# Optimization experiments

Hardware: AMD Instinct MI355X
Metric: run time of the kernel (lower is better)

The kernel has to match this reference:

```python
import jax, jax.numpy as jnp
import numpy as np

H = 1024      # hidden_size
V = 50257     # output_size (vocab)
L = 40        # max_length (attention span)
NL = 2        # num_layers


def setup_inputs() -> dict:
    key = jax.random.key(0)
    ks = jax.random.split(key, 20)
    s = 0.02
    f32 = jnp.float32
    d = {
        "input_token": jax.random.randint(ks[0], (1,), 0, V),
        "h0": jax.random.normal(ks[1], (NL, 1, H), f32),
        "c0": jax.random.normal(ks[2], (NL, 1, H), f32),
        "encoder_outputs": jax.random.normal(ks[3], (L, 2 * H), f32),
        # parameters (PyTorch Linear convention: y = x @ W.T + b)
        "emb": jax.random.normal(ks[4], (V, H), f32) * s,
        "attn_w": jax.random.normal(ks[5], (L, (NL + 1) * H), f32) * s,
        "attn_b": jnp.zeros((L,), f32),
        "comb_w": jax.random.normal(ks[6], (H, 3 * H), f32) * s,
        "comb_b": jnp.zeros((H,), f32),
        "w_ih0": jax.random.normal(ks[7], (4 * H, H), f32) * s,
        "w_hh0": jax.random.normal(ks[8], (4 * H, H), f32) * s,
        "b_ih0": jnp.zeros((4 * H,), f32),
        "b_hh0": jnp.zeros((4 * H,), f32),
        "w_ih1": jax.random.normal(ks[9], (4 * H, H), f32) * s,
        "w_hh1": jax.random.normal(ks[10], (4 * H, H), f32) * s,
        "b_ih1": jnp.zeros((4 * H,), f32),
        "b_hh1": jnp.zeros((4 * H,), f32),
        "out_w": jax.random.normal(ks[11], (V, H), f32) * s,
        "out_b": jnp.zeros((V,), f32),
    }
    return d


def _lstm_cell(x, h, c, w_ih, w_hh, b_ih, b_hh):
    # PyTorch gate order: i, f, g, o
    g = x @ w_ih.T + b_ih + h @ w_hh.T + b_hh  # [1, 4H]
    i, f, gg, o = jnp.split(g, 4, axis=-1)
    c2 = jax.nn.sigmoid(f) * c + jax.nn.sigmoid(i) * jnp.tanh(gg)
    h2 = jax.nn.sigmoid(o) * jnp.tanh(c2)
    return h2, c2


def reference(input_token, h0, c0, encoder_outputs, emb, attn_w, attn_b,
              comb_w, comb_b, w_ih0, w_hh0, b_ih0, b_hh0, w_ih1, w_hh1,
              b_ih1, b_hh1, out_w, out_b):
    embedded = emb[input_token]  # [1, H] (dropout is identity in eval)
    # attention over encoder positions: input = [embedded ; flattened h]
    attn_in = jnp.concatenate([embedded, h0.reshape(1, -1)], axis=1)  # [1, 3H]
    attn_weights = jax.nn.softmax(attn_in @ attn_w.T + attn_b, axis=1)  # [1, L]
    attn_applied = attn_weights @ encoder_outputs  # [1, 2H]
    x = jnp.concatenate([embedded, attn_applied], axis=1) @ comb_w.T + comb_b
    x = jax.nn.relu(x)  # [1, H]
    # 2-layer LSTM, single time step
    h_l0, c_l0 = _lstm_cell(x, h0[0], c0[0], w_ih0, w_hh0, b_ih0, b_hh0)
    h_l1, c_l1 = _lstm_cell(h_l0, h0[1], c0[1], w_ih1, w_hh1, b_ih1, b_hh1)
    h_new = jnp.stack([h_l0, h_l1])  # [NL, 1, H]
    c_new = jnp.stack([c_l0, c_l1])
    log_probs = jax.nn.log_softmax(h_l1 @ out_w.T + out_b, axis=1)  # [1, V]
    return (log_probs, h_new, c_new, attn_weights)
```

## Files before the change

### kernel.cpp

```cpp
#include <hip/hip_runtime.h>
#include <cmath>

#define H 1024
#define VOCAB 50257
#define LSPAN 40

__device__ inline float wave_reduce(float v) {
    for (int o = 32; o > 0; o >>= 1) v += __shfl_down(v, o, 64);
    return v;
}

__global__ void attn_logits_k(const int* __restrict__ tok,
                              const float* __restrict__ h0,
                              const float* __restrict__ emb,
                              const float* __restrict__ attn_w,
                              const float* __restrict__ attn_b,
                              float* __restrict__ ws_logits,
                              float* __restrict__ ws_xin) {
    const int l = blockIdx.x;
    const int t = threadIdx.x;
    const float* __restrict__ er = emb + (size_t)tok[0] * H;
    const float4* __restrict__ w4 = (const float4*)(attn_w + (size_t)l * 3 * H);
    const float4* __restrict__ e4 = (const float4*)er;
    const float4* __restrict__ h4 = (const float4*)h0;
    float acc = 0.f;
    for (int k = t; k < 768; k += 256) {
        float4 w = w4[k];
        float4 x = (k < 256) ? e4[k] : h4[k - 256];
        acc += w.x * x.x + w.y * x.y + w.z * x.z + w.w * x.w;
    }
    if (l == 0 && t < 256) {
        ((float4*)ws_xin)[t] = e4[t];
    }
    __shared__ float lds[4];
    float s = wave_reduce(acc);
    const int wave = t >> 6, lane = t & 63;
    if (lane == 0) lds[wave] = s;
    __syncthreads();
    if (t == 0) ws_logits[l] = lds[0] + lds[1] + lds[2] + lds[3] + attn_b[l];
}

__global__ void attn_apply_k(const float* __restrict__ ws_logits,
                             const float* __restrict__ enc,
                             float* __restrict__ ws_xin,
                             float* __restrict__ out_attnw) {
    __shared__ float lg[LSPAN];
    const int t = threadIdx.x;
    if (t < LSPAN) lg[t] = ws_logits[t];
    __syncthreads();
    float m = -1e30f;
    for (int l = 0; l < LSPAN; ++l) m = fmaxf(m, lg[l]);
    float denom = 0.f;
    for (int l = 0; l < LSPAN; ++l) denom += expf(lg[l] - m);
    const int j = blockIdx.x * 256 + t;
    float acc = 0.f;
    for (int l = 0; l < LSPAN; ++l) {
        acc += expf(lg[l] - m) * enc[l * 2 * H + j];
    }
    ws_xin[H + j] = acc / denom;
    if (blockIdx.x == 0 && t < LSPAN) out_attnw[t] = expf(lg[t] - m) / denom;
}

__global__ void comb_k(const float* __restrict__ ws_xin,
                       const float* __restrict__ comb_w,
                       const float* __restrict__ comb_b,
                       float* __restrict__ ws_x) {
    const int wave = threadIdx.x >> 6, lane = threadIdx.x & 63;
    const int r = blockIdx.x * 4 + wave;
    const float4* __restrict__ w4 = (const float4*)(comb_w + (size_t)r * 3 * H);
    const float4* __restrict__ x4 = (const float4*)ws_xin;
    float acc = 0.f;
    for (int k = lane; k < 768; k += 64) {
        float4 a = w4[k], b = x4[k];
        acc += a.x * b.x + a.y * b.y + a.z * b.z + a.w * b.w;
    }
    acc = wave_reduce(acc);
    if (lane == 0) ws_x[r] = fmaxf(acc + comb_b[r], 0.f);
}

__global__ void lstm_k(const float* __restrict__ x,
                       const float* __restrict__ hprev,
                       const float* __restrict__ cprev,
                       const float* __restrict__ w_ih,
                       const float* __restrict__ w_hh,
                       const float* __restrict__ b_ih,
                       const float* __restrict__ b_hh,
                       float* __restrict__ h_out,
                       float* __restrict__ c_out) {
    const int wave = threadIdx.x >> 6, lane = threadIdx.x & 63;
    const int j = blockIdx.x;
    const int row = wave * H + j;
    const float4* __restrict__ wi4 = (const float4*)(w_ih + (size_t)row * H);
    const float4* __restrict__ wh4 = (const float4*)(w_hh + (size_t)row * H);
    const float4* __restrict__ x4 = (const float4*)x;
    const float4* __restrict__ h4 = (const float4*)hprev;
    float acc = 0.f;
    for (int k = lane; k < 256; k += 64) {
        float4 a = wi4[k], b = x4[k];
        acc += a.x * b.x + a.y * b.y + a.z * b.z + a.w * b.w;
        float4 c = wh4[k], d = h4[k];
        acc += c.x * d.x + c.y * d.y + c.z * d.z + c.w * d.w;
    }
    acc = wave_reduce(acc);
    __shared__ float g[4];
    if (lane == 0) g[wave] = acc + b_ih[row] + b_hh[row];
    __syncthreads();
    if (threadIdx.x == 0) {
        const float i = g[0], f = g[1], gg = g[2], o = g[3];
        const float si = 1.f / (1.f + expf(-i));
        const float sf = 1.f / (1.f + expf(-f));
        const float so = 1.f / (1.f + expf(-o));
        const float c2 = sf * cprev[j] + si * tanhf(gg);
        const float h2 = so * tanhf(c2);
        c_out[j] = c2;
        h_out[j] = h2;
    }
}

__global__ void out_gemv_k(const float* __restrict__ hvec,
                           const float* __restrict__ out_w,
                           const float* __restrict__ out_b,
                           float* __restrict__ logits,
                           float* __restrict__ stats) {
    __shared__ float4 h4s[256];
    const int t = threadIdx.x;
    h4s[t] = ((const float4*)hvec)[t];
    __syncthreads();
    const int wave = t >> 6, lane = t & 63;
    const int v = blockIdx.x * 4 + wave;
    float val = -1e30f;
    if (v < VOCAB) {
        const float4* __restrict__ w4 = (const float4*)(out_w + (size_t)v * H);
        float acc = 0.f;
        for (int k = lane; k < 256; k += 64) {
            float4 a = w4[k];
            float4 b = h4s[k];
            acc += a.x * b.x + a.y * b.y + a.z * b.z + a.w * b.w;
        }
        acc = wave_reduce(acc);
        val = acc + out_b[v];
    }
    __shared__ float g[4];
    if (lane == 0) {
        g[wave] = val;
        if (v < VOCAB) logits[v] = val;
    }
    __syncthreads();
    if (t == 0) {
        float m = fmaxf(fmaxf(g[0], g[1]), fmaxf(g[2], g[3]));
        float s = 0.f;
        for (int w = 0; w < 4; ++w)
            if (g[w] > -1e29f) s += expf(g[w] - m);
        stats[2 * blockIdx.x] = m;
        stats[2 * blockIdx.x + 1] = s;
    }
}

__global__ void logz_k(const float* __restrict__ stats, int nblocks,
                       float* __restrict__ logz) {
    const int t = threadIdx.x;
    float M = -1e30f, S = 0.f;
    for (int b = t; b < nblocks; b += 256) {
        const float m = stats[2 * b], s = stats[2 * b + 1];
        if (m > M) { S = S * expf(M - m) + s; M = m; }
        else       { S += s * expf(m - M); }
    }
    __shared__ float Ms[256], Ss[256];
    Ms[t] = M; Ss[t] = S;
    __syncthreads();
    for (int stride = 128; stride > 0; stride >>= 1) {
        if (t < stride) {
            const float m1 = Ms[t], s1 = Ss[t];
            const float m2 = Ms[t + stride], s2 = Ss[t + stride];
            const float mm = fmaxf(m1, m2);
            Ms[t] = mm;
            Ss[t] = s1 * expf(m1 - mm) + s2 * expf(m2 - mm);
        }
        __syncthreads();
    }
    if (t == 0) logz[0] = Ms[0] + logf(Ss[0]);
}

__global__ void finalize_k(float* __restrict__ logits,
                           const float* __restrict__ logz) {
    const int v = blockIdx.x * 256 + threadIdx.x;
    if (v < VOCAB) logits[v] -= logz[0];
}

extern "C" void kernel_launch(void* const* d_in, const int* in_sizes, int n_in,
                              void* d_out, int out_size, void* d_ws, size_t ws_size,
                              hipStream_t stream) {
    const int*   tok    = (const int*)d_in[0];
    const float* h0     = (const float*)d_in[1];
    const float* c0     = (const float*)d_in[2];
    const float* enc    = (const float*)d_in[3];
    const float* emb    = (const float*)d_in[4];
    const float* attn_w = (const float*)d_in[5];
    const float* attn_b = (const float*)d_in[6];
    const float* comb_w = (const float*)d_in[7];
    const float* comb_b = (const float*)d_in[8];
    const float* w_ih0  = (const float*)d_in[9];
    const float* w_hh0  = (const float*)d_in[10];
    const float* b_ih0  = (const float*)d_in[11];
    const float* b_hh0  = (const float*)d_in[12];
    const float* w_ih1  = (const float*)d_in[13];
    const float* w_hh1  = (const float*)d_in[14];
    const float* b_ih1  = (const float*)d_in[15];
    const float* b_hh1  = (const float*)d_in[16];
    const float* out_w  = (const float*)d_in[17];
    const float* out_b  = (const float*)d_in[18];

    float* out = (float*)d_out;
    float* ws  = (float*)d_ws;

    float* ws_xin    = ws;
    float* ws_x      = ws + 3072;
    float* ws_logits = ws + 4096;
    float* ws_logz   = ws + 4160;
    float* ws_stats  = ws + 4224;

    float* out_logp  = out;
    float* out_h     = out + VOCAB;
    float* out_c     = out + VOCAB + 2 * H;
    float* out_attnw = out + VOCAB + 4 * H;

    attn_logits_k<<<LSPAN, 256, 0, stream>>>(tok, h0, emb, attn_w, attn_b,
                                             ws_logits, ws_xin);
    attn_apply_k<<<8, 256, 0, stream>>>(ws_logits, enc, ws_xin, out_attnw);
    comb_k<<<256, 256, 0, stream>>>(ws_xin, comb_w, comb_b, ws_x);
    lstm_k<<<H, 256, 0, stream>>>(ws_x, h0, c0, w_ih0, w_hh0, b_ih0, b_hh0,
                                  out_h, out_c);
    lstm_k<<<H, 256, 0, stream>>>(out_h, h0 + H, c0 + H, w_ih1, w_hh1, b_ih1,
                                  b_hh1, out_h + H, out_c + H);
    const int NB5 = (VOCAB + 3) / 4;
    out_gemv_k<<<NB5, 256, 0, stream>>>(out_h + H, out_w, out_b, out_logp,
                                        ws_stats);
    logz_k<<<1, 256, 0, stream>>>(ws_stats, NB5, ws_logz);
    finalize_k<<<(VOCAB + 255) / 256, 256, 0, stream>>>(out_logp, ws_logz);
}
```

Measured before the change: 481.0 us.

## Fuse all decoder stages into one cooperative persistent kernel with grid syncs

Replaces the sequence of separate kernel launches (attention logits, attention apply, combine, two LSTM layers, output GEMV, log-softmax) with a single cooperative kernel of 1024 blocks that separates the stages with grid.sync(). The output projection also folds an online max/sum-exp merge into the GEMV, so the log-softmax normalization needs only one extra pass over the logits. The aim is to remove per-launch overhead and inter-kernel gaps. The cost is grid-wide barriers and many idle blocks in the small stages. The old multi-kernel path remains as a fallback if the cooperative launch fails.

```diff
diff --git a/kernel.cpp b/kernel.cpp
--- a/kernel.cpp
+++ b/kernel.cpp
@@ -1,14 +1,196 @@
 #include <hip/hip_runtime.h>
+#include <hip/hip_cooperative_groups.h>
 #include <cmath>
+
+namespace cg = cooperative_groups;
 
 #define H 1024
 #define VOCAB 50257
 #define LSPAN 40
-
-__device__ inline float wave_reduce(float v) {
+#define GRID 1024
+#define NTHR 256
+
+__device__ __forceinline__ float wave_reduce(float v) {
     for (int o = 32; o > 0; o >>= 1) v += __shfl_down(v, o, 64);
     return v;
 }
+
+__device__ __forceinline__ void lsm_merge(float& M, float& S, float m, float s) {
+    if (m > M) { S = S * expf(M - m) + s; M = m; }
+    else       { S += s * expf(m - M); }
+}
+
+__device__ __forceinline__ void lstm_cell(
+    const int j, const int wave, const int lane, const int tid,
+    const float* __restrict__ x, const float* __restrict__ hprev,
+    const float* __restrict__ cprev,
+    const float* __restrict__ w_ih, const float* __restrict__ w_hh,
+    const float* __restrict__ b_ih, const float* __restrict__ b_hh,
+    float* __restrict__ h_out, float* __restrict__ c_out,
+    float* sred) {
+    const int row = wave * H + j;
+    const float4* __restrict__ wi4 = (const float4*)(w_ih + (size_t)row * H);
+    const float4* __restrict__ wh4 = (const float4*)(w_hh + (size_t)row * H);
+    const float4* __restrict__ x4 = (const float4*)x;
+    const float4* __restrict__ h4 = (const float4*)hprev;
+    float acc = 0.f;
+    for (int k = lane; k < 256; k += 64) {
+        float4 a = wi4[k], b = x4[k];
+        acc += a.x * b.x + a.y * b.y + a.z * b.z + a.w * b.w;
+        float4 c = wh4[k], d = h4[k];
+        acc += c.x * d.x + c.y * d.y + c.z * d.z + c.w * d.w;
+    }
+    acc = wave_reduce(acc);
+    if (lane == 0) sred[wave] = acc + b_ih[row] + b_hh[row];
+    __syncthreads();
+    if (tid == 0) {
+        const float i = sred[0], f = sred[1], gg = sred[2], o = sred[3];
+        const float si = 1.f / (1.f + expf(-i));
+        const float sf = 1.f / (1.f + expf(-f));
+        const float so = 1.f / (1.f + expf(-o));
+        const float c2 = sf * cprev[j] + si * tanhf(gg);
+        c_out[j] = c2;
+        h_out[j] = so * tanhf(c2);
+    }
+}
+
+__global__ __launch_bounds__(NTHR, 4) void mega_k(
+    const int* __restrict__ tok, const float* __restrict__ h0,
+    const float* __restrict__ c0, const float* __restrict__ enc,
+    const float* __restrict__ emb, const float* __restrict__ attn_w,
+    const float* __restrict__ attn_b, const float* __restrict__ comb_w,
+    const float* __restrict__ comb_b,
+    const float* __restrict__ w_ih0, const float* __restrict__ w_hh0,
+    const float* __restrict__ b_ih0, const float* __restrict__ b_hh0,
+    const float* __restrict__ w_ih1, const float* __restrict__ w_hh1,
+    const float* __restrict__ b_ih1, const float* __restrict__ b_hh1,
+    const float* __restrict__ out_w, const float* __restrict__ out_b,
+    float* __restrict__ out, float* __restrict__ ws) {
+    cg::grid_group grid = cg::this_grid();
+    const int bid = blockIdx.x, tid = threadIdx.x;
+    const int wave = tid >> 6, lane = tid & 63;
+
+    float* ws_xin   = ws;
+    float* ws_x     = ws + 3072;
+    float* ws_lg    = ws + 4096;
+    float* ws_stats = ws + 4224;
+
+    float* out_logp  = out;
+    float* out_h     = out + VOCAB;
+    float* out_c     = out + VOCAB + 2 * H;
+    float* out_attnw = out + VOCAB + 4 * H;
+
+    __shared__ float4 sh4[256];
+    __shared__ float sA[256];
+    __shared__ float sB[256];
+    __shared__ float slg[LSPAN];
+
+    if (bid < LSPAN) {
+        const float* __restrict__ er = emb + (size_t)tok[0] * H;
+        const float4* __restrict__ w4 = (const float4*)(attn_w + (size_t)bid * 3 * H);
+        const float4* __restrict__ e4 = (const float4*)er;
+        const float4* __restrict__ h4 = (const float4*)h0;
+        float acc = 0.f;
+        for (int k = tid; k < 768; k += NTHR) {
+            float4 w = w4[k];
+            float4 x = (k < 256) ? e4[k] : h4[k - 256];
+            acc += w.x * x.x + w.y * x.y + w.z * x.z + w.w * x.w;
+        }
+        if (bid == 0) ((float4*)ws_xin)[tid] = e4[tid];
+        float s = wave_reduce(acc);
+        if (lane == 0) sA[wave] = s;
+        __syncthreads();
+        if (tid == 0) ws_lg[bid] = sA[0] + sA[1] + sA[2] + sA[3] + attn_b[bid];
+    }
+    grid.sync();
+
+    if (bid < 8) {
+        if (tid < LSPAN) slg[tid] = ws_lg[tid];
+        __syncthreads();
+        float m = -1e30f;
+        for (int l = 0; l < LSPAN; ++l) m = fmaxf(m, slg[l]);
+        float denom = 0.f;
+        for (int l = 0; l < LSPAN; ++l) denom += expf(slg[l] - m);
+        const int j = bid * NTHR + tid;
+        float acc = 0.f;
+        for (int l = 0; l < LSPAN; ++l) acc += expf(slg[l] - m) * enc[l * 2 * H + j];
+        ws_xin[H + j] = acc / denom;
+        if (bid == 0 && tid < LSPAN) out_attnw[tid] = expf(slg[tid] - m) / denom;
+    }
+    grid.sync();
+
+    if (bid < 256) {
+        const int r = bid * 4 + wave;
+        const float4* __restrict__ w4 = (const float4*)(comb_w + (size_t)r * 3 * H);
+        const float4* __restrict__ x4 = (const float4*)ws_xin;
+        float acc = 0.f;
+        for (int k = lane; k < 768; k += 64) {
+            float4 a = w4[k], b = x4[k];
+            acc += a.x * b.x + a.y * b.y + a.z * b.z + a.w * b.w;
+        }
+        acc = wave_reduce(acc);
+        if (lane == 0) ws_x[r] = fmaxf(acc + comb_b[r], 0.f);
+    }
+    grid.sync();
+
+    lstm_cell(bid, wave, lane, tid, ws_x, h0, c0, w_ih0, w_hh0, b_ih0, b_hh0,
+              out_h, out_c, sA);
+    grid.sync();
+
+    lstm_cell(bid, wave, lane, tid, out_h, h0 + H, c0 + H, w_ih1, w_hh1, b_ih1,
+              b_hh1, out_h + H, out_c + H, sA);
+    grid.sync();
+
+    sh4[tid] = ((const float4*)(out_h + H))[tid];
+    __syncthreads();
+    float M = -1e30f, S = 0.f;
+    for (int v = bid * 4 + wave; v < VOCAB; v += GRID * 4) {
+        const float4* __restrict__ w4 = (const float4*)(out_w + (size_t)v * H);
+        float acc = 0.f;
+        #pragma unroll
+        for (int k = lane; k < 256; k += 64) {
+            float4 a = w4[k];
+            float4 b = sh4[k];
+            acc += a.x * b.x + a.y * b.y + a.z * b.z + a.w * b.w;
+        }
+        acc = wave_reduce(acc);
+        if (lane == 0) {
+            const float val = acc + out_b[v];
+            out_logp[v] = val;
+            lsm_merge(M, S, val, 1.f);
+        }
+    }
+    if (lane == 0) { sA[wave] = M; sB[wave] = S; }
+    __syncthreads();
+    if (tid == 0) {
+        float Mb = sA[0], Sb = sB[0];
+        for (int w = 1; w < 4; ++w) lsm_merge(Mb, Sb, sA[w], sB[w]);
+        ws_stats[2 * bid] = Mb;
+        ws_stats[2 * bid + 1] = Sb;
+    }
+    grid.sync();
+
+    float M2 = -1e30f, S2 = 0.f;
+    for (int b = tid; b < GRID; b += NTHR)
+        lsm_merge(M2, S2, ws_stats[2 * b], ws_stats[2 * b + 1]);
+    sA[tid] = M2;
+    sB[tid] = S2;
+    __syncthreads();
+    for (int stride = 128; stride > 0; stride >>= 1) {
+        if (tid < stride) {
+            const float m1 = sA[tid], s1 = sB[tid];
+            const float m2 = sA[tid + stride], s2 = sB[tid + stride];
+            const float mm = fmaxf(m1, m2);
+            sA[tid] = mm;
+            sB[tid] = s1 * expf(m1 - mm) + s2 * expf(m2 - mm);
+        }
+        __syncthreads();
+    }
+    const float logZ = sA[0] + logf(sB[0]);
+    for (int v = bid * NTHR + tid; v < VOCAB; v += GRID * NTHR)
+        out_logp[v] -= logZ;
+}
+
 
 __global__ void attn_logits_k(const int* __restrict__ tok,
                               const float* __restrict__ h0,
@@ -29,9 +211,7 @@
         float4 x = (k < 256) ? e4[k] : h4[k - 256];
         acc += w.x * x.x + w.y * x.y + w.z * x.z + w.w * x.w;
     }
-    if (l == 0 && t < 256) {
-        ((float4*)ws_xin)[t] = e4[t];
-    }
+    if (l == 0 && t < 256) ((float4*)ws_xin)[t] = e4[t];
     __shared__ float lds[4];
     float s = wave_reduce(acc);
     const int wave = t >> 6, lane = t & 63;
@@ -54,9 +234,7 @@
     for (int l = 0; l < LSPAN; ++l) denom += expf(lg[l] - m);
     const int j = blockIdx.x * 256 + t;
     float acc = 0.f;
-    for (int l = 0; l < LSPAN; ++l) {
-        acc += expf(lg[l] - m) * enc[l * 2 * H + j];
-    }
+    for (int l = 0; l < LSPAN; ++l) acc += expf(lg[l] - m) * enc[l * 2 * H + j];
     ws_xin[H + j] = acc / denom;
     if (blockIdx.x == 0 && t < LSPAN) out_attnw[t] = expf(lg[t] - m) / denom;
 }
@@ -88,33 +266,9 @@
                        float* __restrict__ h_out,
                        float* __restrict__ c_out) {
     const int wave = threadIdx.x >> 6, lane = threadIdx.x & 63;
-    const int j = blockIdx.x;
-    const int row = wave * H + j;
-    const float4* __restrict__ wi4 = (const float4*)(w_ih + (size_t)row * H);
-    const float4* __restrict__ wh4 = (const float4*)(w_hh + (size_t)row * H);
-    const float4* __restrict__ x4 = (const float4*)x;
-    const float4* __restrict__ h4 = (const float4*)hprev;
-    float acc = 0.f;
-    for (int k = lane; k < 256; k += 64) {
-        float4 a = wi4[k], b = x4[k];
-        acc += a.x * b.x + a.y * b.y + a.z * b.z + a.w * b.w;
-        float4 c = wh4[k], d = h4[k];
-        acc += c.x * d.x + c.y * d.y + c.z * d.z + c.w * d.w;
-    }
-    acc = wave_reduce(acc);
     __shared__ float g[4];
-    if (lane == 0) g[wave] = acc + b_ih[row] + b_hh[row];
-    __syncthreads();
-    if (threadIdx.x == 0) {
-        const float i = g[0], f = g[1], gg = g[2], o = g[3];
-        const float si = 1.f / (1.f + expf(-i));
-        const float sf = 1.f / (1.f + expf(-f));
-        const float so = 1.f / (1.f + expf(-o));
-        const float c2 = sf * cprev[j] + si * tanhf(gg);
-        const float h2 = so * tanhf(c2);
-        c_out[j] = c2;
-        h_out[j] = h2;
-    }
+    lstm_cell(blockIdx.x, wave, lane, threadIdx.x, x, hprev, cprev, w_ih, w_hh,
+              b_ih, b_hh, h_out, c_out, g);
 }
 
 __global__ void out_gemv_k(const float* __restrict__ hvec,
@@ -213,6 +367,16 @@
     float* out = (float*)d_out;
     float* ws  = (float*)d_ws;
 
+    void* params[] = {
+        (void*)&tok, (void*)&h0, (void*)&c0, (void*)&enc, (void*)&emb,
+        (void*)&attn_w, (void*)&attn_b, (void*)&comb_w, (void*)&comb_b,
+        (void*)&w_ih0, (void*)&w_hh0, (void*)&b_ih0, (void*)&b_hh0,
+        (void*)&w_ih1, (void*)&w_hh1, (void*)&b_ih1, (void*)&b_hh1,
+        (void*)&out_w, (void*)&out_b, (void*)&out, (void*)&ws};
+    hipError_t err = hipLaunchCooperativeKernel((const void*)mega_k, dim3(GRID),
+                                                dim3(NTHR), params, 0, stream);
+    if (err == hipSuccess) return;
+
     float* ws_xin    = ws;
     float* ws_x      = ws + 3072;
     float* ws_logits = ws + 4096;
```

Measured after the change: 1.135 ms. 2.36x slower.

## Fuse attention kernels and merge logsumexp reduction into finalize kernel

Applied to the files above, without the earlier changes.

Merges the attention-logit and attention-apply kernels into one kernel, where each of the 8 blocks recomputes all 40 logits redundantly with one wave per row. The vocab GEMV now uses 1024-thread blocks covering 16 rows, with an online max/sum merge per block. The separate logz kernel is folded into finalize: every one of 50 blocks re-reduces all per-block stats before subtracting. This cuts the launch count from 8 to 6 in exchange for redundant recomputation inside blocks.

```diff
diff --git a/kernel.cpp b/kernel.cpp
--- a/kernel.cpp
+++ b/kernel.cpp
@@ -4,61 +4,55 @@
 #define H 1024
 #define VOCAB 50257
 #define LSPAN 40
-
-__device__ inline float wave_reduce(float v) {
+#define NB5 3142
+#define NBF 50
+
+__device__ __forceinline__ float wave_reduce(float v) {
     for (int o = 32; o > 0; o >>= 1) v += __shfl_down(v, o, 64);
     return v;
 }
 
-__global__ void attn_logits_k(const int* __restrict__ tok,
-                              const float* __restrict__ h0,
-                              const float* __restrict__ emb,
-                              const float* __restrict__ attn_w,
-                              const float* __restrict__ attn_b,
-                              float* __restrict__ ws_logits,
-                              float* __restrict__ ws_xin) {
-    const int l = blockIdx.x;
-    const int t = threadIdx.x;
+__device__ __forceinline__ void lsm_merge(float& M, float& S, float m, float s) {
+    if (m > M) { S = S * expf(M - m) + s; M = m; }
+    else       { S += s * expf(m - M); }
+}
+
+__global__ void attn_k(const int* __restrict__ tok,
+                       const float* __restrict__ h0,
+                       const float* __restrict__ emb,
+                       const float* __restrict__ attn_w,
+                       const float* __restrict__ attn_b,
+                       const float* __restrict__ enc,
+                       float* __restrict__ ws_xin,
+                       float* __restrict__ out_attnw) {
+    const int t = threadIdx.x, bid = blockIdx.x;
+    const int wave = t >> 6, lane = t & 63;
+    __shared__ float slg[LSPAN];
     const float* __restrict__ er = emb + (size_t)tok[0] * H;
-    const float4* __restrict__ w4 = (const float4*)(attn_w + (size_t)l * 3 * H);
     const float4* __restrict__ e4 = (const float4*)er;
     const float4* __restrict__ h4 = (const float4*)h0;
+    for (int l = wave; l < LSPAN; l += 4) {
+        const float4* __restrict__ w4 = (const float4*)(attn_w + (size_t)l * 3 * H);
+        float acc = 0.f;
+        for (int k = lane; k < 768; k += 64) {
+            float4 w = w4[k];
+            float4 x = (k < 256) ? e4[k] : h4[k - 256];
+            acc += w.x * x.x + w.y * x.y + w.z * x.z + w.w * x.w;
+        }
+        acc = wave_reduce(acc);
+        if (lane == 0) slg[l] = acc + attn_b[l];
+    }
+    if (bid == 0) ((float4*)ws_xin)[t] = e4[t];
+    __syncthreads();
+    float m = -1e30f;
+    for (int l = 0; l < LSPAN; ++l) m = fmaxf(m, slg[l]);
+    float denom = 0.f;
+    for (int l = 0; l < LSPAN; ++l) denom += expf(slg[l] - m);
+    const int j = bid * 256 + t;
     float acc = 0.f;
-    for (int k = t; k < 768; k += 256) {
-        float4 w = w4[k];
-        float4 x = (k < 256) ? e4[k] : h4[k - 256];
-        acc += w.x * x.x + w.y * x.y + w.z * x.z + w.w * x.w;
-    }
-    if (l == 0 && t < 256) {
-        ((float4*)ws_xin)[t] = e4[t];
-    }
-    __shared__ float lds[4];
-    float s = wave_reduce(acc);
-    const int wave = t >> 6, lane = t & 63;
-    if (lane == 0) lds[wave] = s;
-    __syncthreads();
-    if (t == 0) ws_logits[l] = lds[0] + lds[1] + lds[2] + lds[3] + attn_b[l];
-}
-
-__global__ void attn_apply_k(const float* __restrict__ ws_logits,
-                             const float* __restrict__ enc,
-                             float* __restrict__ ws_xin,
-                             float* __restrict__ out_attnw) {
-    __shared__ float lg[LSPAN];
-    const int t = threadIdx.x;
-    if (t < LSPAN) lg[t] = ws_logits[t];
-    __syncthreads();
-    float m = -1e30f;
-    for (int l = 0; l < LSPAN; ++l) m = fmaxf(m, lg[l]);
-    float denom = 0.f;
-    for (int l = 0; l < LSPAN; ++l) denom += expf(lg[l] - m);
-    const int j = blockIdx.x * 256 + t;
-    float acc = 0.f;
-    for (int l = 0; l < LSPAN; ++l) {
-        acc += expf(lg[l] - m) * enc[l * 2 * H + j];
-    }
+    for (int l = 0; l < LSPAN; ++l) acc += expf(slg[l] - m) * enc[l * 2 * H + j];
     ws_xin[H + j] = acc / denom;
-    if (blockIdx.x == 0 && t < LSPAN) out_attnw[t] = expf(lg[t] - m) / denom;
+    if (bid == 0 && t < LSPAN) out_attnw[t] = expf(slg[t] - m) / denom;
 }
 
 __global__ void comb_k(const float* __restrict__ ws_xin,
@@ -117,74 +111,74 @@
     }
 }
 
-__global__ void out_gemv_k(const float* __restrict__ hvec,
-                           const float* __restrict__ out_w,
-                           const float* __restrict__ out_b,
-                           float* __restrict__ logits,
-                           float* __restrict__ stats) {
-    __shared__ float4 h4s[256];
+__global__ __launch_bounds__(1024, 2) void out_gemv_k(
+    const float* __restrict__ hvec,
+    const float* __restrict__ out_w,
+    const float* __restrict__ out_b,
+    float* __restrict__ logits,
+    float* __restrict__ stats) {
+    __shared__ float4 sh4[256];
+    __shared__ float sM[16], sS[16];
     const int t = threadIdx.x;
-    h4s[t] = ((const float4*)hvec)[t];
+    if (t < 256) sh4[t] = ((const float4*)hvec)[t];
     __syncthreads();
     const int wave = t >> 6, lane = t & 63;
-    const int v = blockIdx.x * 4 + wave;
-    float val = -1e30f;
+    const int v = blockIdx.x * 16 + wave;
+    float M = -1e30f, S = 0.f;
     if (v < VOCAB) {
         const float4* __restrict__ w4 = (const float4*)(out_w + (size_t)v * H);
         float acc = 0.f;
-        for (int k = lane; k < 256; k += 64) {
+        #pragma unroll
+        for (int i = 0; i < 4; ++i) {
+            const int k = lane + i * 64;
             float4 a = w4[k];
-            float4 b = h4s[k];
+            float4 b = sh4[k];
             acc += a.x * b.x + a.y * b.y + a.z * b.z + a.w * b.w;
         }
         acc = wave_reduce(acc);
-        val = acc + out_b[v];
-    }
-    __shared__ float g[4];
-    if (lane == 0) {
-        g[wave] = val;
-        if (v < VOCAB) logits[v] = val;
-    }
+        if (lane == 0) {
+            const float val = acc + out_b[v];
+            logits[v] = val;
+            M = val;
+            S = 1.f;
+        }
+    }
+    if (lane == 0) { sM[wave] = M; sS[wave] = S; }
     __syncthreads();
     if (t == 0) {
-        float m = fmaxf(fmaxf(g[0], g[1]), fmaxf(g[2], g[3]));
-        float s = 0.f;
-        for (int w = 0; w < 4; ++w)
-            if (g[w] > -1e29f) s += expf(g[w] - m);
-        stats[2 * blockIdx.x] = m;
-        stats[2 * blockIdx.x + 1] = s;
-    }
-}
-
-__global__ void logz_k(const float* __restrict__ stats, int nblocks,
-                       float* __restrict__ logz) {
+        float Mb = sM[0], Sb = sS[0];
+        for (int w = 1; w < 16; ++w) lsm_merge(Mb, Sb, sM[w], sS[w]);
+        stats[2 * blockIdx.x] = Mb;
+        stats[2 * blockIdx.x + 1] = Sb;
+    }
+}
+
+__global__ __launch_bounds__(1024) void finalize_k(
+    const float* __restrict__ stats,
+    float* __restrict__ logits) {
     const int t = threadIdx.x;
+    const int wave = t >> 6, lane = t & 63;
     float M = -1e30f, S = 0.f;
-    for (int b = t; b < nblocks; b += 256) {
-        const float m = stats[2 * b], s = stats[2 * b + 1];
-        if (m > M) { S = S * expf(M - m) + s; M = m; }
-        else       { S += s * expf(m - M); }
-    }
-    __shared__ float Ms[256], Ss[256];
-    Ms[t] = M; Ss[t] = S;
-    __syncthreads();
-    for (int stride = 128; stride > 0; stride >>= 1) {
-        if (t < stride) {
-            const float m1 = Ms[t], s1 = Ss[t];
-            const float m2 = Ms[t + stride], s2 = Ss[t + stride];
-            const float mm = fmaxf(m1, m2);
-            Ms[t] = mm;
-            Ss[t] = s1 * expf(m1 - mm) + s2 * expf(m2 - mm);
-        }
-        __syncthreads();
-    }
-    if (t == 0) logz[0] = Ms[0] + logf(Ss[0]);
-}
-
-__global__ void finalize_k(float* __restrict__ logits,
-                           const float* __restrict__ logz) {
-    const int v = blockIdx.x * 256 + threadIdx.x;
-    if (v < VOCAB) logits[v] -= logz[0];
+    for (int b = t; b < NB5; b += 1024)
+        lsm_merge(M, S, stats[2 * b], stats[2 * b + 1]);
+    for (int o = 32; o > 0; o >>= 1) {
+        const float m2 = __shfl_down(M, o, 64);
+        const float s2 = __shfl_down(S, o, 64);
+        lsm_merge(M, S, m2, s2);
+    }
+    __shared__ float sM[16], sS[16];
+    __shared__ float slz;
+    if (lane == 0) { sM[wave] = M; sS[wave] = S; }
+    __syncthreads();
+    if (t == 0) {
+        float Mb = sM[0], Sb = sS[0];
+        for (int w = 1; w < 16; ++w) lsm_merge(Mb, Sb, sM[w], sS[w]);
+        slz = Mb + logf(Sb);
+    }
+    __syncthreads();
+    const float lz = slz;
+    const int v = blockIdx.x * 1024 + t;
+    if (v < VOCAB) logits[v] -= lz;
 }
 
 extern "C" void kernel_launch(void* const* d_in, const int* in_sizes, int n_in,
@@ -213,28 +207,23 @@
     float* out = (float*)d_out;
     float* ws  = (float*)d_ws;
 
-    float* ws_xin    = ws;
-    float* ws_x      = ws + 3072;
-    float* ws_logits = ws + 4096;
-    float* ws_logz   = ws + 4160;
-    float* ws_stats  = ws + 4224;
+    float* ws_xin   = ws;
+    float* ws_x     = ws + 3072;
+    float* ws_stats = ws + 4224;
 
     float* out_logp  = out;
     float* out_h     = out + VOCAB;
     float* out_c     = out + VOCAB + 2 * H;
     float* out_attnw = out + VOCAB + 4 * H;
 
-    attn_logits_k<<<LSPAN, 256, 0, stream>>>(tok, h0, emb, attn_w, attn_b,
-                                             ws_logits, ws_xin);
-    attn_apply_k<<<8, 256, 0, stream>>>(ws_logits, enc, ws_xin, out_attnw);
+    attn_k<<<8, 256, 0, stream>>>(tok, h0, emb, attn_w, attn_b, enc,
+                                  ws_xin, out_attnw);
     comb_k<<<256, 256, 0, stream>>>(ws_xin, comb_w, comb_b, ws_x);
     lstm_k<<<H, 256, 0, stream>>>(ws_x, h0, c0, w_ih0, w_hh0, b_ih0, b_hh0,
                                   out_h, out_c);
     lstm_k<<<H, 256, 0, stream>>>(out_h, h0 + H, c0 + H, w_ih1, w_hh1, b_ih1,
                                   b_hh1, out_h + H, out_c + H);
-    const int NB5 = (VOCAB + 3) / 4;
-    out_gemv_k<<<NB5, 256, 0, stream>>>(out_h + H, out_w, out_b, out_logp,
-                                        ws_stats);
-    logz_k<<<1, 256, 0, stream>>>(ws_stats, NB5, ws_logz);
-    finalize_k<<<(VOCAB + 255) / 256, 256, 0, stream>>>(out_logp, ws_logz);
-}
+    out_gemv_k<<<NB5, 1024, 0, stream>>>(out_h + H, out_w, out_b, out_logp,
+                                         ws_stats);
+    finalize_k<<<NBF, 1024, 0, stream>>>(ws_stats, out_logp);
+}
```

Measured after the change: 508.1 us. +5.6%, slower.
